# Optimization experiments

Hardware: AMD Instinct MI355X
Metric: run time of the kernel (lower is better)

Reference implementation:

```python
import jax, jax.numpy as jnp
import numpy as np

B = 16
NT, NH_, NW_, T_, H_, W_ = 4, 14, 14, 4, 1, 1
C = 768
NHEAD = 12
HD = C // NHEAD
SCALE = 1.0 / float(np.sqrt(HD))
TT = NT * T_            # 16 temporal slices
T2 = TT // 2            # 8 after even/odd split
HW = (NH_ * H_) * (NW_ * W_)  # 196 spatial tokens
TOKENS = NT * NH_ * NW_ * T_ * H_ * W_


def setup_inputs() -> dict:
    key = jax.random.key(0)
    ks = jax.random.split(key, 14)
    def lin(k, din, dout):
        return jax.random.normal(k, (din, dout), jnp.float32) * 0.02
    return {
        "x_in": jax.random.normal(ks[0], (B, TOKENS, C), jnp.float32),
        "Wq_d": lin(ks[1], C, C),      "bq_d": jnp.zeros((C,), jnp.float32),
        "Wkv_a": lin(ks[2], C, 2 * C), "bkv_a": jnp.zeros((2 * C,), jnp.float32),
        "Wq_a": lin(ks[3], C, C),      "bq_a": jnp.zeros((C,), jnp.float32),
        "Wkv_d": lin(ks[4], C, 2 * C), "bkv_d": jnp.zeros((2 * C,), jnp.float32),
        "Wp_d": lin(ks[5], C, C),      "bp_d": jnp.zeros((C,), jnp.float32),
        "Wp_a": lin(ks[6], C, C),      "bp_a": jnp.zeros((C,), jnp.float32),
    }


def _cross_attn(q_x, kv_x, Wq, bq, Wkv, bkv):
    # q_x, kv_x: (b, t, hw, c)
    b, t, hw, c = q_x.shape
    q = (q_x @ Wq + bq).reshape(b, t, hw, NHEAD, HD)
    kv = (kv_x @ Wkv + bkv).reshape(b, t, hw, 2, NHEAD, HD)
    k, v = kv[..., 0, :, :], kv[..., 1, :, :]
    s = jnp.einsum('btqhd,btkhd->bthqk', q, k) * SCALE
    p = jax.nn.softmax(s, axis=-1)
    o = jnp.einsum('bthqk,btkhd->btqhd', p, v)
    return o.reshape(b, t, hw, c)


def reference(x_in, Wq_d, bq_d, Wkv_a, bkv_a, Wq_a, bq_a, Wkv_d, bkv_d,
              Wp_d, bp_d, Wp_a, bp_a):
    b = x_in.shape[0]
    # einops: b (nt nh nw t h w) c -> b (nt t) (nh h) (nw w) c
    x = x_in.reshape(b, NT, NH_, NW_, T_, H_, W_, C)
    x = x.transpose(0, 1, 4, 2, 5, 3, 6, 7).reshape(b, TT, NH_ * H_, NW_ * W_, C)
    x_skip = x                                   # (b, TT, h, w, c)
    x = x.reshape(b, TT, HW, C)                  # (b, TT, hw, c)
    x_a = x[:, 0::2]                             # (b, T2, hw, c) approx
    x_d = x[:, 1::2]                             # (b, T2, hw, c) detail

    # detail cross-attends to approx, subtract-update
    _d = _cross_attn(x_d, x_a, Wq_d, bq_d, Wkv_a, bkv_a)
    _d = jax.nn.gelu(_d @ Wp_d + bp_d, approximate=False)
    x_d = x_d - _d
    # approx cross-attends to updated detail, add-update
    _a = _cross_attn(x_a, x_d, Wq_a, bq_a, Wkv_d, bkv_d)
    _a = jax.nn.gelu(_a @ Wp_a + bp_a, approximate=False)
    x_a = x_a + _a

    # relaxed_constrain: pooled-skip minus channel-mean of x_a
    xs = x_skip.reshape(b, TT, HW, C)
    pooled = xs.reshape(b, T2, 2, HW, C).mean(axis=2)   # avg_pool2d (2,1)
    pool_a = pooled.mean(axis=-1) - x_a.mean(axis=-1)   # (b, T2, hw)

    # SSL=False: mean over channels, keepdim (torch layout b,1,t,hw)
    x_d_out = x_d.mean(axis=-1)[:, None, :, :]          # (b, 1, T2, hw)
    return (pool_a, x_d_out)
```

## Files before the change

### kernel.cpp

```cpp
#include <hip/hip_runtime.h>

typedef __bf16 bf16;
typedef __attribute__((ext_vector_type(8))) __bf16 bf16x8;
typedef __attribute__((ext_vector_type(4))) __bf16 bf16x4;
typedef __attribute__((ext_vector_type(2))) __bf16 bf16x2;
typedef __attribute__((ext_vector_type(4))) float f32x4;
typedef __attribute__((ext_vector_type(4))) unsigned int u32x4;

#define TOKENS 3136
#define CC 768
#define S196 196
#define M_ROWS 25088
#define BATCH 16

__device__ __forceinline__ float bf2f(bf16 x) { return (float)x; }
__device__ __forceinline__ bf16 f2bf(float x) { return (bf16)x; }

__device__ __forceinline__ float gelu_exact(float x) {
    return 0.5f * x * (1.0f + erff(x * 0.70710678118654752f));
}

__device__ __forceinline__ unsigned int packbf(float a, float b) {
    bf16x2 v; v[0] = (bf16)a; v[1] = (bf16)b;
    return __builtin_bit_cast(unsigned int, v);
}

#define GLOAD_LDS16(gp, lp) \
    __builtin_amdgcn_global_load_lds((const __attribute__((address_space(1))) void*)(gp), \
                                     (__attribute__((address_space(3))) void*)(lp), 16, 0, 0)

__global__ __launch_bounds__(256)
void transpose_w(const float* __restrict__ W, bf16* __restrict__ Wt, int K, int N)
{
    __shared__ float tle[32][33];
    int k0 = blockIdx.x * 32, n0 = blockIdx.y * 32;
    int tx = threadIdx.x & 31, ty = threadIdx.x >> 5;
    for (int r = ty; r < 32; r += 8)
        tle[r][tx] = W[(long)(k0 + r) * N + n0 + tx];
    __syncthreads();
    for (int r = ty; r < 32; r += 8)
        Wt[(long)(n0 + r) * K + k0 + tx] = f2bf(tle[tx][r]);
}

__global__ __launch_bounds__(256)
void conv_bias(const float* b0, const float* b1, const float* b2,
               const float* b3, const float* b4, const float* b5,
               bf16* __restrict__ dst)
{
    const float* srcs[6] = {b0, b1, b2, b3, b4, b5};
    const int sizes[6]   = {768, 1536, 768, 1536, 768, 768};
    const int offs[6]    = {0, 768, 2304, 3072, 4608, 5376};
    int which = blockIdx.x;
    const float* s = srcs[which];
    int n = sizes[which];
    bf16* d = dst + offs[which];
    for (int i = threadIdx.x; i < n; i += 256)
        d[i] = f2bf(s[i]);
}

__global__ __launch_bounds__(256)
void reorder_split(const float* __restrict__ x_in, bf16* __restrict__ xa,
                   bf16* __restrict__ xd)
{
    long idx = (long)blockIdx.x * 256 + threadIdx.x;
    const long total = (long)BATCH * 16 * S196 * 96;
    if (idx >= total) return;
    int  c8  = (int)(idx % 96) * 8;
    long row = idx / 96;
    int  s   = (int)(row % S196);
    long r2  = row / S196;
    int  tt  = (int)(r2 & 15);
    int  b   = (int)(r2 >> 4);
    int  nt  = tt >> 2, t = tt & 3;
    int  nh  = s / 14,  nw = s % 14;
    long src  = ((long)b * TOKENS + ((nt * 14 + nh) * 14 + nw) * 4 + t) * CC + c8;
    bf16* dst = (tt & 1) ? xd : xa;
    long doff = ((long)(b * 8 + (tt >> 1)) * S196 + s) * CC + c8;
    const float* sp = x_in + src;
    f32x4 a = *(const f32x4*)sp;
    f32x4 c = *(const f32x4*)(sp + 4);
    bf16x8 v;
    v[0] = f2bf(a[0]); v[1] = f2bf(a[1]); v[2] = f2bf(a[2]); v[3] = f2bf(a[3]);
    v[4] = f2bf(c[0]); v[5] = f2bf(c[1]); v[6] = f2bf(c[2]); v[7] = f2bf(c[3]);
    *(bf16x8*)(dst + doff) = v;
}

__device__ __forceinline__ float row_sum768(const bf16* __restrict__ p, int lane)
{
    float s = 0.f;
    bf16x8 v = *(const bf16x8*)(p + lane * 8);
    #pragma unroll
    for (int j = 0; j < 8; ++j) s += bf2f(v[j]);
    if (lane < 32) {
        bf16x8 w = *(const bf16x8*)(p + 512 + lane * 8);
        #pragma unroll
        for (int j = 0; j < 8; ++j) s += bf2f(w[j]);
    }
    #pragma unroll
    for (int off = 32; off; off >>= 1) s += __shfl_xor(s, off, 64);
    return s;
}

__global__ __launch_bounds__(256)
void pool_ad(const bf16* __restrict__ xa, const bf16* __restrict__ xd,
             float* __restrict__ pool0)
{
    int id = blockIdx.x * 4 + (threadIdx.x >> 6);
    int lane = threadIdx.x & 63;
    float sa = row_sum768(xa + (long)id * CC, lane);
    float sd = row_sum768(xd + (long)id * CC, lane);
    if (lane == 0) pool0[id] = (sa + sd) * (0.5f / 768.0f);
}

__global__ __launch_bounds__(256)
void out_final(const bf16* __restrict__ xa, const bf16* __restrict__ xd,
               const float* __restrict__ pool0, float* __restrict__ out)
{
    int id = blockIdx.x * 4 + (threadIdx.x >> 6);
    int lane = threadIdx.x & 63;
    float sa = row_sum768(xa + (long)id * CC, lane);
    float sd = row_sum768(xd + (long)id * CC, lane);
    if (lane == 0) {
        out[id]          = pool0[id] - sa * (1.0f / 768.0f);
        out[M_ROWS + id] = sd * (1.0f / 768.0f);
    }
}

template<int EPI>
__global__ __launch_bounds__(512, 2)
void gemm_bt(const bf16* __restrict__ A, const bf16* __restrict__ Bt,
             const bf16* __restrict__ bias, const bf16* __restrict__ res,
             bf16* __restrict__ C, int ldc, int mTiles, int nTiles)
{
    constexpr int K = 768, NKT = 12;
    __shared__ alignas(16) bf16 sA[4][8192];
    __shared__ alignas(16) bf16 sB[4][8192];
    const int tid  = threadIdx.x;
    const int lane = tid & 63, wave = tid >> 6;
    const int wm   = wave >> 2, wn = wave & 3;
    const int quad = lane >> 4, l16 = lane & 15;

    const int GM = 8;
    int pid   = blockIdx.x;
    int group = GM * nTiles;
    int gid   = pid / group;
    int rem   = pid - gid * group;
    int first = gid * GM;
    int gm    = (mTiles - first < GM) ? (mTiles - first) : GM;
    int bm    = first + rem % gm;
    int bn    = rem / gm;

    const long m0 = (long)bm * 256;
    const long n0 = (long)bn * 256;

    const int fl    = (l16 & 3) ^ (l16 >> 2);
    const int aoffA = (wm * 128 + l16) * 32 + ((quad ^ fl) * 8);
    const int aoffB = (wn * 64  + l16) * 32 + ((quad ^ fl) * 8);

    const int  cch = (lane & 3) ^ ((lane >> 2) & 3) ^ quad;
    const int  r0  = wave * 16 + (lane >> 2);
    const int  r1  = (8 + wave) * 16 + (lane >> 2);
    const long so0 = (long)r0 * K + cch * 8;
    const long so1 = (long)r1 * K + cch * 8;
    const int  ld0 = wave * 512, ld1 = (8 + wave) * 512;
    const bf16* Ab = A  + m0 * K;
    const bf16* Bb = Bt + n0 * K;

    f32x4 acc[8][4] = {};

    #define STG_A(slot, koff) do { \
        GLOAD_LDS16(Ab + (koff) + so0, &sA[slot][ld0]); \
        GLOAD_LDS16(Ab + (koff) + so1, &sA[slot][ld1]); } while (0)
    #define STG_B(slot, koff) do { \
        GLOAD_LDS16(Bb + (koff) + so0, &sB[slot][ld0]); \
        GLOAD_LDS16(Bb + (koff) + so1, &sB[slot][ld1]); } while (0)

    STG_A(0, 0);  STG_B(0, 0);
    STG_A(1, 32); STG_B(1, 32);
    STG_A(2, 64); STG_B(2, 64);
    asm volatile("s_waitcnt vmcnt(8)" ::: "memory");
    __builtin_amdgcn_s_barrier();

    #define MFMA16(H) do { \
        __builtin_amdgcn_s_setprio(1); \
        _Pragma("unroll") \
        for (int mf = 0; mf < 4; ++mf) \
            _Pragma("unroll") \
            for (int nf = 0; nf < 4; ++nf) \
                acc[(H)*4 + mf][nf] = __builtin_amdgcn_mfma_f32_16x16x32_bf16( \
                    a[mf], b[nf], acc[(H)*4 + mf][nf], 0, 0, 0); \
        __builtin_amdgcn_s_setprio(0); } while (0)

    #pragma unroll 2
    for (int t = 0; t < NKT; ++t) {
        const int sl0 = (2 * t) & 3;
        const int sl1 = (2 * t + 1) & 3;
        const int slN = (2 * t + 3) & 3;
        bf16x8 a[4], b[4];

        #pragma unroll
        for (int mf = 0; mf < 4; ++mf) a[mf] = *(const bf16x8*)(&sA[sl0][mf * 512 + aoffA]);
        #pragma unroll
        for (int nf = 0; nf < 4; ++nf) b[nf] = *(const bf16x8*)(&sB[sl0][nf * 512 + aoffB]);
        if (t + 1 < NKT) STG_A(slN, (t + 1) * 64 + 32);
        __builtin_amdgcn_s_barrier();
        __builtin_amdgcn_sched_barrier(0);
        MFMA16(0);
        __builtin_amdgcn_s_barrier();

        #pragma unroll
        for (int mf = 0; mf < 4; ++mf) a[mf] = *(const bf16x8*)(&sA[sl0][2048 + mf * 512 + aoffA]);
        if (t + 1 < NKT) STG_B(slN, (t + 1) * 64 + 32);
        __builtin_amdgcn_s_barrier();
        __builtin_amdgcn_sched_barrier(0);
        MFMA16(1);
        if (t + 1 < NKT) asm volatile("s_waitcnt vmcnt(8)" ::: "memory");
        else             asm volatile("s_waitcnt vmcnt(0)" ::: "memory");
        __builtin_amdgcn_s_barrier();

        #pragma unroll
        for (int mf = 0; mf < 4; ++mf) a[mf] = *(const bf16x8*)(&sA[sl1][mf * 512 + aoffA]);
        #pragma unroll
        for (int nf = 0; nf < 4; ++nf) b[nf] = *(const bf16x8*)(&sB[sl1][nf * 512 + aoffB]);
        if (t + 2 < NKT) STG_A(sl0, (t + 2) * 64);
        __builtin_amdgcn_s_barrier();
        __builtin_amdgcn_sched_barrier(0);
        MFMA16(0);
        __builtin_amdgcn_s_barrier();

        #pragma unroll
        for (int mf = 0; mf < 4; ++mf) a[mf] = *(const bf16x8*)(&sA[sl1][2048 + mf * 512 + aoffA]);
        if (t + 2 < NKT) STG_B(sl0, (t + 2) * 64);
        __builtin_amdgcn_s_barrier();
        __builtin_amdgcn_sched_barrier(0);
        MFMA16(1);
        if      (t + 2 < NKT) asm volatile("s_waitcnt vmcnt(8)" ::: "memory");
        else if (t + 1 < NKT) asm volatile("s_waitcnt vmcnt(4)" ::: "memory");
        __builtin_amdgcn_s_barrier();
    }
    #undef STG_A
    #undef STG_B
    #undef MFMA16

    #pragma unroll
    for (int mf = 0; mf < 8; ++mf) {
        #pragma unroll
        for (int nf = 0; nf < 4; ++nf) {
            int mg = (int)m0 + wm * 128 + mf * 16 + quad * 4;
            int ng = (int)n0 + wn * 64 + nf * 16 + l16;
            float bn_ = bf2f(bias[ng]);
            #pragma unroll
            for (int r = 0; r < 4; ++r) {
                float x = acc[mf][nf][r] + bn_;
                long off = (long)(mg + r) * ldc + ng;
                if (EPI == 0)      C[off] = f2bf(x);
                else if (EPI == 1) C[off] = f2bf(bf2f(res[off]) - gelu_exact(x));
                else               C[off] = f2bf(bf2f(res[off]) + gelu_exact(x));
            }
        }
    }
}

#define KSTR 72
#define VSTR 264

__global__ __launch_bounds__(256)
void attn_mfma(const bf16* __restrict__ Q, int ldq,
               const bf16* __restrict__ KV, int ldkv,
               bf16* __restrict__ O)
{
    const int h  = blockIdx.x;
    const int bj = blockIdx.y;
    __shared__ alignas(16) bf16 Ks[208 * KSTR];
    __shared__ alignas(16) bf16 Vt[64 * VSTR];
    const int tid = threadIdx.x, lane = tid & 63, wave = tid >> 6;
    const int quad = lane >> 4, l16 = lane & 15;

    const bf16* qg = Q  + (long)bj * S196 * ldq  + h * 64;
    const bf16* kg = KV + (long)bj * S196 * ldkv + h * 64;
    const bf16* vg = kg + CC;

    for (int i = tid; i < 208 * 8; i += 256) {
        int r = i >> 3, c8 = (i & 7) * 8;
        bf16x8 v = {};
        if (r < S196) v = *(const bf16x8*)(kg + (long)r * ldkv + c8);
        *(bf16x8*)(Ks + r * KSTR + c8) = v;
    }
    for (int i = tid; i < 256 * 8; i += 256) {
        int g   = i >> 6;
        int c8  = (g & 7) * 8;
        int tok = (g >> 3) * 64 + (i & 63);
        bf16x8 v = {};
        if (tok < S196) v = *(const bf16x8*)(vg + (long)tok * ldkv + c8);
        #pragma unroll
        for (int j = 0; j < 8; ++j)
            Vt[(c8 + j) * VSTR + tok] = v[j];
    }
    __syncthreads();

    for (int qt = wave; qt < 13; qt += 4) {
        int qrow = qt * 16 + l16; if (qrow > 195) qrow = 195;
        const bf16* qrp = qg + (long)qrow * ldq + quad * 8;
        bf16x8 qf0 = *(const bf16x8*)(qrp);
        bf16x8 qf1 = *(const bf16x8*)(qrp + 32);

        f32x4 st[13];
        #pragma unroll
        for (int rt = 0; rt < 13; ++rt) st[rt] = (f32x4){0.f, 0.f, 0.f, 0.f};
        #pragma unroll
        for (int rt = 0; rt < 13; ++rt) {
            const bf16* kb = Ks + (rt * 16 + l16) * KSTR + quad * 8;
            bf16x8 kf0 = *(const bf16x8*)(kb);
            bf16x8 kf1 = *(const bf16x8*)(kb + 32);
            st[rt] = __builtin_amdgcn_mfma_f32_16x16x32_bf16(kf0, qf0, st[rt], 0, 0, 0);
            st[rt] = __builtin_amdgcn_mfma_f32_16x16x32_bf16(kf1, qf1, st[rt], 0, 0, 0);
        }

        const float SC = 0.125f;
        #pragma unroll
        for (int rt = 0; rt < 13; ++rt) {
            st[rt][0] *= SC; st[rt][1] *= SC; st[rt][2] *= SC; st[rt][3] *= SC;
        }
        if (quad != 0)
            st[12] = (f32x4){-1e30f, -1e30f, -1e30f, -1e30f};

        float m = -1e30f;
        #pragma unroll
        for (int rt = 0; rt < 13; ++rt)
            m = fmaxf(m, fmaxf(fmaxf(st[rt][0], st[rt][1]), fmaxf(st[rt][2], st[rt][3])));
        m = fmaxf(m, __shfl_xor(m, 16, 64));
        m = fmaxf(m, __shfl_xor(m, 32, 64));
        float sum = 0.f;
        #pragma unroll
        for (int rt = 0; rt < 13; ++rt) {
            st[rt][0] = __expf(st[rt][0] - m);
            st[rt][1] = __expf(st[rt][1] - m);
            st[rt][2] = __expf(st[rt][2] - m);
            st[rt][3] = __expf(st[rt][3] - m);
            sum += st[rt][0] + st[rt][1] + st[rt][2] + st[rt][3];
        }
        sum += __shfl_xor(sum, 16, 64);
        sum += __shfl_xor(sum, 32, 64);
        float inv = 1.0f / sum;

        unsigned int pk[13][2];
        #pragma unroll
        for (int rt = 0; rt < 13; ++rt) {
            pk[rt][0] = packbf(st[rt][0] * inv, st[rt][1] * inv);
            pk[rt][1] = packbf(st[rt][2] * inv, st[rt][3] * inv);
        }

        f32x4 ot[4];
        #pragma unroll
        for (int dt = 0; dt < 4; ++dt) ot[dt] = (f32x4){0.f, 0.f, 0.f, 0.f};
        #pragma unroll
        for (int c = 0; c < 7; ++c) {
            u32x4 fp;
            #pragma unroll
            for (int jp = 0; jp < 4; ++jp) {
                int jh = jp >> 1, rp = jp & 1;
                int srcb = ((((quad & 1) << 1) + jh) << 6) | (l16 << 2);
                int a = __builtin_amdgcn_ds_bpermute(srcb, (int)pk[2 * c][rp]);
                int b = (c < 6) ? __builtin_amdgcn_ds_bpermute(srcb, (int)pk[2 * c + 1][rp]) : 0;
                fp[jp] = (quad >> 1) ? (unsigned int)b : (unsigned int)a;
            }
            bf16x8 pB = __builtin_bit_cast(bf16x8, fp);
            #pragma unroll
            for (int dt = 0; dt < 4; ++dt) {
                bf16x8 vf = *(const bf16x8*)(Vt + (dt * 16 + l16) * VSTR + c * 32 + quad * 8);
                ot[dt] = __builtin_amdgcn_mfma_f32_16x16x32_bf16(vf, pB, ot[dt], 0, 0, 0);
            }
        }

        int token = qt * 16 + l16;
        if (token < S196) {
            bf16* op = O + ((long)bj * S196 + token) * CC + h * 64 + quad * 4;
            #pragma unroll
            for (int dt = 0; dt < 4; ++dt) {
                bf16x4 v;
                v[0] = f2bf(ot[dt][0]); v[1] = f2bf(ot[dt][1]);
                v[2] = f2bf(ot[dt][2]); v[3] = f2bf(ot[dt][3]);
                *(bf16x4*)(op + dt * 16) = v;
            }
        }
    }
}

extern "C" void kernel_launch(void* const* d_in, const int* in_sizes, int n_in,
                              void* d_out, int out_size, void* d_ws, size_t ws_size,
                              hipStream_t stream)
{
    const float* x_in  = (const float*)d_in[0];
    const float* Wq_d  = (const float*)d_in[1];
    const float* bq_d  = (const float*)d_in[2];
    const float* Wkv_a = (const float*)d_in[3];
    const float* bkv_a = (const float*)d_in[4];
    const float* Wq_a  = (const float*)d_in[5];
    const float* bq_a  = (const float*)d_in[6];
    const float* Wkv_d = (const float*)d_in[7];
    const float* bkv_d = (const float*)d_in[8];
    const float* Wp_d  = (const float*)d_in[9];
    const float* bp_d  = (const float*)d_in[10];
    const float* Wp_a  = (const float*)d_in[11];
    const float* bp_a  = (const float*)d_in[12];
    float* out = (float*)d_out;

    char* w = (char*)d_ws;
    auto alloc = [&](size_t elems) {
        bf16* p = (bf16*)w;
        w += ((elems * 2 + 255) / 256) * 256;
        return p;
    };
    bf16* biasAll = alloc(6144);
    bf16* WtQd  = alloc((size_t)768 * 768);
    bf16* WtACat= alloc((size_t)2304 * 768);
    bf16* WtKd  = alloc((size_t)1536 * 768);
    bf16* WtPd  = alloc((size_t)768 * 768);
    bf16* WtPa  = alloc((size_t)768 * 768);
    bf16* xa    = alloc((size_t)M_ROWS * 768);
    bf16* xd    = alloc((size_t)M_ROWS * 768);
    bf16* Qb    = alloc((size_t)M_ROWS * 768);
    bf16* QKVa  = alloc((size_t)M_ROWS * 2304);
    bf16* Ob    = alloc((size_t)M_ROWS * 768);
    float* pool0 = (float*)w; w += ((size_t)M_ROWS * 4 + 255) / 256 * 256;

    dim3 blk(256);
    dim3 blk512(512);
    transpose_w<<<dim3(24, 24), blk, 0, stream>>>(Wq_d,  WtQd, 768, 768);
    transpose_w<<<dim3(24, 48), blk, 0, stream>>>(Wkv_a, WtACat, 768, 1536);
    transpose_w<<<dim3(24, 24), blk, 0, stream>>>(Wq_a,  WtACat + (size_t)1536 * 768, 768, 768);
    transpose_w<<<dim3(24, 48), blk, 0, stream>>>(Wkv_d, WtKd, 768, 1536);
    transpose_w<<<dim3(24, 24), blk, 0, stream>>>(Wp_d,  WtPd, 768, 768);
    transpose_w<<<dim3(24, 24), blk, 0, stream>>>(Wp_a,  WtPa, 768, 768);
    conv_bias<<<dim3(6), blk, 0, stream>>>(bq_d, bkv_a, bq_a, bkv_d, bp_d, bp_a, biasAll);

    long total_chunks = (long)BATCH * 16 * S196 * 96;
    int  rblocks = (int)((total_chunks + 255) / 256);
    reorder_split<<<rblocks, blk, 0, stream>>>(x_in, xa, xd);
    pool_ad<<<M_ROWS / 4, blk, 0, stream>>>(xa, xd, pool0);

    const bf16* Bq_d   = biasAll;
    const bf16* Bkva_qa= biasAll + 768;
    const bf16* Bkv_d  = biasAll + 3072;
    const bf16* Bp_d   = biasAll + 4608;
    const bf16* Bp_a   = biasAll + 5376;

    gemm_bt<0><<<dim3(98 * 3), blk512, 0, stream>>>(xd, WtQd,  Bq_d,    nullptr, Qb,   768,  98, 3);
    gemm_bt<0><<<dim3(98 * 9), blk512, 0, stream>>>(xa, WtACat, Bkva_qa, nullptr, QKVa, 2304, 98, 9);
    attn_mfma<<<dim3(12, 128), blk, 0, stream>>>(Qb, 768, QKVa, 2304, Ob);
    gemm_bt<1><<<dim3(98 * 3), blk512, 0, stream>>>(Ob, WtPd, Bp_d, xd, xd, 768, 98, 3);

    gemm_bt<0><<<dim3(98 * 6), blk512, 0, stream>>>(xd, WtKd, Bkv_d, nullptr, QKVa, 2304, 98, 6);
    attn_mfma<<<dim3(12, 128), blk, 0, stream>>>(QKVa + 1536, 2304, QKVa, 2304, Ob);
    gemm_bt<2><<<dim3(98 * 3), blk512, 0, stream>>>(Ob, WtPa, Bp_a, xa, xa, 768, 98, 3);

    out_final<<<M_ROWS / 4, blk, 0, stream>>>(xa, xd, pool0, out);
}
```

Before: 936.8 us.

## Use 128x128 GEMM tiles for small GEMMs and remap XCDs in 256 kernel

Adds a simple single-buffered 128x128-tile GEMM kernel and uses it for the Q, output-projection and detail-KV GEMMs. This raises the workgroup count, so the small-N GEMMs fill more compute units. The 256-tile kernel gains XCD-aware block remapping and a new LDS swizzle layout, and its scheduling barriers are removed. The new kernel has no multi-stage prefetch and may suffer LDS bank conflicts.

```diff
diff --git a/kernel.cpp b/kernel.cpp
--- a/kernel.cpp
+++ b/kernel.cpp
@@ -127,20 +127,20 @@
 }
 
 template<int EPI>
-__global__ __launch_bounds__(512, 2)
-void gemm_bt(const bf16* __restrict__ A, const bf16* __restrict__ Bt,
-             const bf16* __restrict__ bias, const bf16* __restrict__ res,
-             bf16* __restrict__ C, int ldc, int mTiles, int nTiles)
-{
-    constexpr int K = 768, NKT = 12;
-    __shared__ alignas(16) bf16 sA[4][8192];
-    __shared__ alignas(16) bf16 sB[4][8192];
+__global__ __launch_bounds__(256)
+void gemm_bt128(const bf16* __restrict__ A, const bf16* __restrict__ Bt,
+                const bf16* __restrict__ bias, const bf16* __restrict__ res,
+                bf16* __restrict__ C, int ldc, int K, int mTiles, int nTiles)
+{
+    constexpr int BM = 128, BK = 32;
+    __shared__ alignas(16) bf16 sA[BM * BK];
+    __shared__ alignas(16) bf16 sB[BM * BK];
     const int tid  = threadIdx.x;
     const int lane = tid & 63, wave = tid >> 6;
-    const int wm   = wave >> 2, wn = wave & 3;
+    const int wm   = wave >> 1, wn = wave & 1;
     const int quad = lane >> 4, l16 = lane & 15;
 
-    const int GM = 8;
+    const int GM = 16;
     int pid   = blockIdx.x;
     int group = GM * nTiles;
     int gid   = pid / group;
@@ -150,30 +150,113 @@
     int bm    = first + rem % gm;
     int bn    = rem / gm;
 
+    const long m0 = (long)bm * BM;
+    const long n0 = (long)bn * BM;
+
+    f32x4 acc[4][4] = {};
+
+    for (int kt = 0; kt < K; kt += BK) {
+        if (kt) __syncthreads();
+        #pragma unroll
+        for (int c = 0; c < 2; ++c) {
+            int ci = (wave * 2 + c) * 64 + lane;
+            int r  = ci >> 2, kc = ci & 3;
+            const bf16* ga = A  + (m0 + r) * K + kt + kc * 8;
+            const bf16* gb = Bt + (n0 + r) * K + kt + kc * 8;
+            bf16* la = sA + (wave * 2 + c) * 512;
+            bf16* lb = sB + (wave * 2 + c) * 512;
+            GLOAD_LDS16(ga, la);
+            GLOAD_LDS16(gb, lb);
+        }
+        __syncthreads();
+
+        bf16x8 af[4], bfr[4];
+        #pragma unroll
+        for (int mi = 0; mi < 4; ++mi)
+            af[mi] = *(const bf16x8*)(sA + (wm * 64 + mi * 16 + l16) * BK + quad * 8);
+        #pragma unroll
+        for (int ni = 0; ni < 4; ++ni)
+            bfr[ni] = *(const bf16x8*)(sB + (wn * 64 + ni * 16 + l16) * BK + quad * 8);
+        #pragma unroll
+        for (int mi = 0; mi < 4; ++mi)
+            #pragma unroll
+            for (int ni = 0; ni < 4; ++ni)
+                acc[mi][ni] = __builtin_amdgcn_mfma_f32_16x16x32_bf16(af[mi], bfr[ni], acc[mi][ni], 0, 0, 0);
+    }
+
+    #pragma unroll
+    for (int mi = 0; mi < 4; ++mi) {
+        #pragma unroll
+        for (int ni = 0; ni < 4; ++ni) {
+            int mg = (int)m0 + wm * 64 + mi * 16 + quad * 4;
+            int ng = (int)n0 + wn * 64 + ni * 16 + l16;
+            float bn_ = bf2f(bias[ng]);
+            #pragma unroll
+            for (int r = 0; r < 4; ++r) {
+                float x = acc[mi][ni][r] + bn_;
+                long off = (long)(mg + r) * ldc + ng;
+                if (EPI == 0)      C[off] = f2bf(x);
+                else if (EPI == 1) C[off] = f2bf(bf2f(res[off]) - gelu_exact(x));
+                else               C[off] = f2bf(bf2f(res[off]) + gelu_exact(x));
+            }
+        }
+    }
+}
+
+template<int EPI>
+__global__ __launch_bounds__(512, 2)
+void gemm_bt256(const bf16* __restrict__ A, const bf16* __restrict__ Bt,
+                const bf16* __restrict__ bias, const bf16* __restrict__ res,
+                bf16* __restrict__ C, int ldc, int mTiles, int nTiles)
+{
+    constexpr int K = 768, NKT = 12;
+    __shared__ alignas(16) bf16 sA[4][8192];
+    __shared__ alignas(16) bf16 sB[4][8192];
+    const int tid  = threadIdx.x;
+    const int lane = tid & 63, wave = tid >> 6;
+    const int wm   = wave >> 2, wn = wave & 3;
+    const int quad = lane >> 4, l16 = lane & 15;
+
+    int nwg  = (int)gridDim.x;
+    int orig = (int)blockIdx.x;
+    int q8 = nwg >> 3, r8 = nwg & 7, xcd = orig & 7;
+    int pid = (xcd < r8 ? xcd * (q8 + 1) : r8 * (q8 + 1) + (xcd - r8) * q8)
+              + (orig >> 3);
+
+    const int GM = 8;
+    int group = GM * nTiles;
+    int gid   = pid / group;
+    int rem   = pid - gid * group;
+    int first = gid * GM;
+    int gm    = (mTiles - first < GM) ? (mTiles - first) : GM;
+    int bm    = first + rem % gm;
+    int bn    = rem / gm;
+
     const long m0 = (long)bm * 256;
     const long n0 = (long)bn * 256;
 
-    const int fl    = (l16 & 3) ^ (l16 >> 2);
-    const int aoffA = (wm * 128 + l16) * 32 + ((quad ^ fl) * 8);
-    const int aoffB = (wn * 64  + l16) * 32 + ((quad ^ fl) * 8);
-
-    const int  cch = (lane & 3) ^ ((lane >> 2) & 3) ^ quad;
-    const int  r0  = wave * 16 + (lane >> 2);
-    const int  r1  = (8 + wave) * 16 + (lane >> 2);
-    const long so0 = (long)r0 * K + cch * 8;
-    const long so1 = (long)r1 * K + cch * 8;
-    const int  ld0 = wave * 512, ld1 = (8 + wave) * 512;
+    const int lh  = l16 >> 1;
+    const int px  = ((l16 & 1) << 2) | quad;
+    const int pxl = (px ^ lh) * 8;
+    const int aoffA = (wm * 64 + lh) * 64 + pxl;
+    const int aoffB = (wn * 32 + lh) * 64 + pxl;
+
+    const int  cg  = (tid & 7) ^ ((tid >> 3) & 7);
+    const int  rr  = ((tid >> 3) << 1) + (cg >> 2);
+    const long soA0 = (long)rr * K + (cg & 3) * 8;
+    const long soA1 = (long)(128 + rr) * K + (cg & 3) * 8;
+    const int  ldd0 = wave * 512, ldd1 = 4096 + wave * 512;
     const bf16* Ab = A  + m0 * K;
     const bf16* Bb = Bt + n0 * K;
 
     f32x4 acc[8][4] = {};
 
     #define STG_A(slot, koff) do { \
-        GLOAD_LDS16(Ab + (koff) + so0, &sA[slot][ld0]); \
-        GLOAD_LDS16(Ab + (koff) + so1, &sA[slot][ld1]); } while (0)
+        GLOAD_LDS16(Ab + (koff) + soA0, &sA[slot][ldd0]); \
+        GLOAD_LDS16(Ab + (koff) + soA1, &sA[slot][ldd1]); } while (0)
     #define STG_B(slot, koff) do { \
-        GLOAD_LDS16(Bb + (koff) + so0, &sB[slot][ld0]); \
-        GLOAD_LDS16(Bb + (koff) + so1, &sB[slot][ld1]); } while (0)
+        GLOAD_LDS16(Bb + (koff) + soA0, &sB[slot][ldd0]); \
+        GLOAD_LDS16(Bb + (koff) + soA1, &sB[slot][ldd1]); } while (0)
 
     STG_A(0, 0);  STG_B(0, 0);
     STG_A(1, 32); STG_B(1, 32);
@@ -204,7 +287,6 @@
         for (int nf = 0; nf < 4; ++nf) b[nf] = *(const bf16x8*)(&sB[sl0][nf * 512 + aoffB]);
         if (t + 1 < NKT) STG_A(slN, (t + 1) * 64 + 32);
         __builtin_amdgcn_s_barrier();
-        __builtin_amdgcn_sched_barrier(0);
         MFMA16(0);
         __builtin_amdgcn_s_barrier();
 
@@ -212,7 +294,6 @@
         for (int mf = 0; mf < 4; ++mf) a[mf] = *(const bf16x8*)(&sA[sl0][2048 + mf * 512 + aoffA]);
         if (t + 1 < NKT) STG_B(slN, (t + 1) * 64 + 32);
         __builtin_amdgcn_s_barrier();
-        __builtin_amdgcn_sched_barrier(0);
         MFMA16(1);
         if (t + 1 < NKT) asm volatile("s_waitcnt vmcnt(8)" ::: "memory");
         else             asm volatile("s_waitcnt vmcnt(0)" ::: "memory");
@@ -224,7 +305,6 @@
         for (int nf = 0; nf < 4; ++nf) b[nf] = *(const bf16x8*)(&sB[sl1][nf * 512 + aoffB]);
         if (t + 2 < NKT) STG_A(sl0, (t + 2) * 64);
         __builtin_amdgcn_s_barrier();
-        __builtin_amdgcn_sched_barrier(0);
         MFMA16(0);
         __builtin_amdgcn_s_barrier();
 
@@ -232,7 +312,6 @@
         for (int mf = 0; mf < 4; ++mf) a[mf] = *(const bf16x8*)(&sA[sl1][2048 + mf * 512 + aoffA]);
         if (t + 2 < NKT) STG_B(sl0, (t + 2) * 64);
         __builtin_amdgcn_s_barrier();
-        __builtin_amdgcn_sched_barrier(0);
         MFMA16(1);
         if      (t + 2 < NKT) asm volatile("s_waitcnt vmcnt(8)" ::: "memory");
         else if (t + 1 < NKT) asm volatile("s_waitcnt vmcnt(4)" ::: "memory");
@@ -445,14 +524,14 @@
     const bf16* Bp_d   = biasAll + 4608;
     const bf16* Bp_a   = biasAll + 5376;
 
-    gemm_bt<0><<<dim3(98 * 3), blk512, 0, stream>>>(xd, WtQd,  Bq_d,    nullptr, Qb,   768,  98, 3);
-    gemm_bt<0><<<dim3(98 * 9), blk512, 0, stream>>>(xa, WtACat, Bkva_qa, nullptr, QKVa, 2304, 98, 9);
+    gemm_bt128<0><<<dim3(196 * 6), blk, 0, stream>>>(xd, WtQd, Bq_d, nullptr, Qb, 768, 768, 196, 6);
+    gemm_bt256<0><<<dim3(98 * 9), blk512, 0, stream>>>(xa, WtACat, Bkva_qa, nullptr, QKVa, 2304, 98, 9);
     attn_mfma<<<dim3(12, 128), blk, 0, stream>>>(Qb, 768, QKVa, 2304, Ob);
-    gemm_bt<1><<<dim3(98 * 3), blk512, 0, stream>>>(Ob, WtPd, Bp_d, xd, xd, 768, 98, 3);
-
-    gemm_bt<0><<<dim3(98 * 6), blk512, 0, stream>>>(xd, WtKd, Bkv_d, nullptr, QKVa, 2304, 98, 6);
+    gemm_bt128<1><<<dim3(196 * 6), blk, 0, stream>>>(Ob, WtPd, Bp_d, xd, xd, 768, 768, 196, 6);
+
+    gemm_bt128<0><<<dim3(196 * 12), blk, 0, stream>>>(xd, WtKd, Bkv_d, nullptr, QKVa, 2304, 768, 196, 12);
     attn_mfma<<<dim3(12, 128), blk, 0, stream>>>(QKVa + 1536, 2304, QKVa, 2304, Ob);
-    gemm_bt<2><<<dim3(98 * 3), blk512, 0, stream>>>(Ob, WtPa, Bp_a, xa, xa, 768, 98, 3);
+    gemm_bt128<2><<<dim3(196 * 6), blk, 0, stream>>>(Ob, WtPa, Bp_a, xa, xa, 768, 768, 196, 6);
 
     out_final<<<M_ROWS / 4, blk, 0, stream>>>(xa, xd, pool0, out);
 }
```

New measurement: 864.0 us. -7.8%, faster.
